# Performance work log

Measured on AMD Instinct MI355X. Metric: run time of the kernel, lower is better.

## Reference

```python
import jax, jax.numpy as jnp
import numpy as np

B = 4096
D_IN = 1024
D_H = 1024


def setup_inputs() -> dict:
    key = jax.random.key(0)
    ks = jax.random.split(key, 11)
    s = 1.0 / np.sqrt(D_IN + D_H)  # torch nn.Linear default init scale
    def w(k):
        return jax.random.uniform(k, (D_H, D_IN + D_H), jnp.float32, -s, s)
    def b(k):
        return jax.random.uniform(k, (D_H,), jnp.float32, -s, s)
    return {
        "inputs": jax.random.normal(ks[0], (B, D_IN), jnp.float32),
        "h_prev": jax.random.normal(ks[1], (B, D_H), jnp.float32),
        "c_prev": jax.random.normal(ks[2], (B, D_H), jnp.float32),
        "W_i": w(ks[3]), "b_i": b(ks[4]),
        "W_f": w(ks[5]), "b_f": b(ks[6]),
        "W_c": w(ks[7]), "b_c": b(ks[8]),
        "W_o": w(ks[9]), "b_o": b(ks[10]),
    }


def reference(inputs, h_prev, c_prev, W_i, b_i, W_f, b_f, W_c, b_c, W_o, b_o):
    combined = jnp.concatenate([inputs, h_prev], axis=1)  # [B, D_IN+D_H]
    # Fuse the four gate projections into one GEMM: [B, 4*D_H]
    W = jnp.concatenate([W_i, W_f, W_c, W_o], axis=0)      # [4*D_H, D_IN+D_H]
    bvec = jnp.concatenate([b_i, b_f, b_c, b_o], axis=0)   # [4*D_H]
    z = combined @ W.T + bvec
    zi, zf, zc, zo = jnp.split(z, 4, axis=1)
    i_gate = jax.nn.sigmoid(zi)
    f_gate = jax.nn.sigmoid(zf)
    c_gate = jnp.tanh(zc)
    o_gate = jax.nn.sigmoid(zo)
    c_next = f_gate * c_prev + i_gate * c_gate
    h_next = o_gate * jnp.tanh(c_next)
    return (h_next, c_next)
```

## Files before the change

### kernel.cpp

```cpp
#include <hip/hip_runtime.h>
#include <hip/hip_bf16.h>
#include <stdint.h>

#define B_SZ 4096
#define D_K  2048
#define DH   1024

#define BM 128
#define BN_H 32
#define BK 64

typedef __attribute__((ext_vector_type(8))) short short8;
typedef __attribute__((ext_vector_type(4))) float floatx4;

__device__ __forceinline__ float fast_sigmoid(float x) {
  return 1.0f / (1.0f + __expf(-x));
}
__device__ __forceinline__ float fast_tanh(float x) {
  return 2.0f / (1.0f + __expf(-2.0f * x)) - 1.0f;
}

__device__ __forceinline__ uint32_t bf16pk(float a, float b) {
  union { float f; uint32_t u; } ua, ub;
  ua.f = a; ub.f = b;
  uint32_t x = ua.u + (0x7FFFu + ((ua.u >> 16) & 1u));
  uint32_t y = ub.u + (0x7FFFu + ((ub.u >> 16) & 1u));
  return (x >> 16) | (y & 0xFFFF0000u);
}

__global__ __launch_bounds__(256) void prep_kernel(
    const float* __restrict__ xin, const float* __restrict__ hprev,
    const float* __restrict__ Wi, const float* __restrict__ Wf,
    const float* __restrict__ Wc, const float* __restrict__ Wo,
    uint32_t* __restrict__ Abf, uint32_t* __restrict__ Wbf)
{
  const int NT = (B_SZ * D_K) / 8;
  int t = blockIdx.x * blockDim.x + threadIdx.x;
  const float* src;
  uint32_t* dst;
  if (t < NT) {
    int idx8 = t * 8;
    int m = idx8 >> 11;
    int k = idx8 & (D_K - 1);
    src = (k < 1024) ? (xin + m * 1024 + k) : (hprev + m * 1024 + (k - 1024));
    dst = Abf + t * 4;
  } else {
    int u = t - NT;
    int idx8 = u * 8;
    int n = idx8 >> 11;
    int k = idx8 & (D_K - 1);
    int g = n >> 10, h = n & 1023;
    const float* wsrc = (g == 0) ? Wi : (g == 1) ? Wf : (g == 2) ? Wc : Wo;
    src = wsrc + (size_t)h * D_K + k;
    dst = Wbf + u * 4;
  }
  float4 f0 = *(const float4*)(src);
  float4 f1 = *(const float4*)(src + 4);
  uint4 v;
  v.x = bf16pk(f0.x, f0.y);
  v.y = bf16pk(f0.z, f0.w);
  v.z = bf16pk(f1.x, f1.y);
  v.w = bf16pk(f1.z, f1.w);
  *(uint4*)dst = v;
}

__global__ __launch_bounds__(256, 3) void lstm_gemm_kernel(
    const __hip_bfloat16* __restrict__ A,
    const __hip_bfloat16* __restrict__ W,
    const float* __restrict__ bi, const float* __restrict__ bfv,
    const float* __restrict__ bc, const float* __restrict__ bo,
    const float* __restrict__ cprev,
    float* __restrict__ out)
{
  __shared__ __align__(16) __hip_bfloat16 lA[BM * BK];
  __shared__ __align__(16) __hip_bfloat16 lB[128 * BK];

  const int m0 = blockIdx.x * BM;
  const int h0 = blockIdx.y * BN_H;
  const int tid = threadIdx.x;
  const int wave = tid >> 6;
  const int lane = tid & 63;
  const int wm = wave >> 1;
  const int wn = wave & 1;

  const int sr = lane >> 3;
  const int pc = lane & 7;
  const int gc = pc ^ sr;

  const __hip_bfloat16* aSrc[4];
  const __hip_bfloat16* bSrc[4];
  __hip_bfloat16* aDst[4];
  __hip_bfloat16* bDst[4];
  #pragma unroll
  for (int j = 0; j < 4; ++j) {
    int row = j * 32 + wave * 8 + sr;
    aSrc[j] = A + (size_t)(m0 + row) * D_K + gc * 8;
    aDst[j] = &lA[row * BK + pc * 8];
    bSrc[j] = W + (size_t)(j * DH + h0 + wave * 8 + sr) * D_K + gc * 8;
    bDst[j] = &lB[row * BK + pc * 8];
  }

  floatx4 acc[4][4];
  #pragma unroll
  for (int i = 0; i < 4; ++i)
    #pragma unroll
    for (int j = 0; j < 4; ++j)
      acc[i][j] = (floatx4){0.f, 0.f, 0.f, 0.f};

  const int fr = lane & 15;
  const int q  = lane >> 4;
  const int key = fr & 7;
  const int cx0 = ((q + 0) ^ key) * 8;
  const int cx1 = ((q + 4) ^ key) * 8;

  for (int kt = 0; kt < D_K; kt += BK) {
    #pragma unroll
    for (int j = 0; j < 4; ++j)
      __builtin_amdgcn_global_load_lds(
          (const __attribute__((address_space(1))) void*)(aSrc[j] + kt),
          (__attribute__((address_space(3))) void*)aDst[j], 16, 0, 0);
    #pragma unroll
    for (int j = 0; j < 4; ++j)
      __builtin_amdgcn_global_load_lds(
          (const __attribute__((address_space(1))) void*)(bSrc[j] + kt),
          (__attribute__((address_space(3))) void*)bDst[j], 16, 0, 0);
    __syncthreads();

    #pragma unroll
    for (int kk = 0; kk < 2; ++kk) {
      const int cx = kk ? cx1 : cx0;
      short8 bfr[4];
      #pragma unroll
      for (int g = 0; g < 4; ++g)
        bfr[g] = *(const short8*)&lB[(g * 32 + wn * 16 + fr) * BK + cx];
      #pragma unroll
      for (int i = 0; i < 4; ++i) {
        short8 af = *(const short8*)&lA[(wm * 64 + i * 16 + fr) * BK + cx];
        acc[i][0] = __builtin_amdgcn_mfma_f32_16x16x32_bf16(af, bfr[0], acc[i][0], 0, 0, 0);
        acc[i][1] = __builtin_amdgcn_mfma_f32_16x16x32_bf16(af, bfr[1], acc[i][1], 0, 0, 0);
        acc[i][2] = __builtin_amdgcn_mfma_f32_16x16x32_bf16(af, bfr[2], acc[i][2], 0, 0, 0);
        acc[i][3] = __builtin_amdgcn_mfma_f32_16x16x32_bf16(af, bfr[3], acc[i][3], 0, 0, 0);
      }
    }
    __syncthreads();
  }

  const int col = lane & 15;
  const int rq = lane >> 4;
  const int h = h0 + wn * 16 + col;
  const float bias_i = bi[h], bias_f = bfv[h], bias_c = bc[h], bias_o = bo[h];
  float* hout = out;
  float* cout = out + (size_t)B_SZ * DH;
  #pragma unroll
  for (int i = 0; i < 4; ++i) {
    int mb = m0 + wm * 64 + i * 16 + rq * 4;
    #pragma unroll
    for (int r = 0; r < 4; ++r) {
      int m = mb + r;
      float zi = acc[i][0][r] + bias_i;
      float zf = acc[i][1][r] + bias_f;
      float zc = acc[i][2][r] + bias_c;
      float zo = acc[i][3][r] + bias_o;
      float ig = fast_sigmoid(zi);
      float fg = fast_sigmoid(zf);
      float cg = fast_tanh(zc);
      float og = fast_sigmoid(zo);
      float cp = cprev[(size_t)m * DH + h];
      float cn = fg * cp + ig * cg;
      float hn = og * fast_tanh(cn);
      hout[(size_t)m * DH + h] = hn;
      cout[(size_t)m * DH + h] = cn;
    }
  }
}

extern "C" void kernel_launch(void* const* d_in, const int* in_sizes, int n_in,
                              void* d_out, int out_size, void* d_ws, size_t ws_size,
                              hipStream_t stream)
{
  const float* xin   = (const float*)d_in[0];
  const float* hprev = (const float*)d_in[1];
  const float* cprev = (const float*)d_in[2];
  const float* Wi    = (const float*)d_in[3];
  const float* bi    = (const float*)d_in[4];
  const float* Wf    = (const float*)d_in[5];
  const float* bfv   = (const float*)d_in[6];
  const float* Wc    = (const float*)d_in[7];
  const float* bc    = (const float*)d_in[8];
  const float* Wo    = (const float*)d_in[9];
  const float* bo    = (const float*)d_in[10];
  float* out = (float*)d_out;

  __hip_bfloat16* Abf = (__hip_bfloat16*)d_ws;
  __hip_bfloat16* Wbf = Abf + (size_t)B_SZ * D_K;

  const int totalThreads = 2 * (B_SZ * D_K / 8);
  prep_kernel<<<totalThreads / 256, 256, 0, stream>>>(
      xin, hprev, Wi, Wf, Wc, Wo, (uint32_t*)Abf, (uint32_t*)Wbf);

  dim3 grid(B_SZ / BM, DH / BN_H);
  lstm_gemm_kernel<<<grid, 256, 0, stream>>>(Abf, Wbf, bi, bfv, bc, bo, cprev, out);
}
```

Before: 208.4 us.

## Double-buffer LDS tiles with BK=32 and remap blocks for XCD locality

```diff
diff --git a/kernel.cpp b/kernel.cpp
--- a/kernel.cpp
+++ b/kernel.cpp
@@ -8,7 +8,7 @@
 
 #define BM 128
 #define BN_H 32
-#define BK 64
+#define BK 32
 
 typedef __attribute__((ext_vector_type(8))) short short8;
 typedef __attribute__((ext_vector_type(4))) float floatx4;
@@ -34,34 +34,32 @@
     const float* __restrict__ Wc, const float* __restrict__ Wo,
     uint32_t* __restrict__ Abf, uint32_t* __restrict__ Wbf)
 {
-  const int NT = (B_SZ * D_K) / 8;
+  const int NT = (B_SZ * D_K) / 4;
   int t = blockIdx.x * blockDim.x + threadIdx.x;
   const float* src;
   uint32_t* dst;
   if (t < NT) {
-    int idx8 = t * 8;
-    int m = idx8 >> 11;
-    int k = idx8 & (D_K - 1);
-    src = (k < 1024) ? (xin + m * 1024 + k) : (hprev + m * 1024 + (k - 1024));
-    dst = Abf + t * 4;
+    int idx4 = t * 4;
+    int m = idx4 >> 11;
+    int k = idx4 & (D_K - 1);
+    src = (k < 1024) ? (xin + (size_t)m * 1024 + k)
+                     : (hprev + (size_t)m * 1024 + (k - 1024));
+    dst = Abf + (size_t)t * 2;
   } else {
     int u = t - NT;
-    int idx8 = u * 8;
-    int n = idx8 >> 11;
-    int k = idx8 & (D_K - 1);
+    int idx4 = u * 4;
+    int n = idx4 >> 11;
+    int k = idx4 & (D_K - 1);
     int g = n >> 10, h = n & 1023;
     const float* wsrc = (g == 0) ? Wi : (g == 1) ? Wf : (g == 2) ? Wc : Wo;
     src = wsrc + (size_t)h * D_K + k;
-    dst = Wbf + u * 4;
-  }
-  float4 f0 = *(const float4*)(src);
-  float4 f1 = *(const float4*)(src + 4);
-  uint4 v;
-  v.x = bf16pk(f0.x, f0.y);
-  v.y = bf16pk(f0.z, f0.w);
-  v.z = bf16pk(f1.x, f1.y);
-  v.w = bf16pk(f1.z, f1.w);
-  *(uint4*)dst = v;
+    dst = Wbf + (size_t)u * 2;
+  }
+  float4 f = *(const float4*)src;
+  uint2 v;
+  v.x = bf16pk(f.x, f.y);
+  v.y = bf16pk(f.z, f.w);
+  *(uint2*)dst = v;
 }
 
 __global__ __launch_bounds__(256, 3) void lstm_gemm_kernel(
@@ -72,32 +70,36 @@
     const float* __restrict__ cprev,
     float* __restrict__ out)
 {
-  __shared__ __align__(16) __hip_bfloat16 lA[BM * BK];
-  __shared__ __align__(16) __hip_bfloat16 lB[128 * BK];
-
-  const int m0 = blockIdx.x * BM;
-  const int h0 = blockIdx.y * BN_H;
+  __shared__ __align__(16) __hip_bfloat16 lA[2][BM * BK];
+  __shared__ __align__(16) __hip_bfloat16 lB[2][128 * BK];
+
+  const int l = blockIdx.x;
+  const int q = l >> 3;
+  const int mIdx = q & 31;
+  const int hIdx = (l & 7) * 4 + (q >> 5);
+  const int m0 = mIdx * BM;
+  const int h0 = hIdx * BN_H;
+
   const int tid = threadIdx.x;
   const int wave = tid >> 6;
   const int lane = tid & 63;
   const int wm = wave >> 1;
   const int wn = wave & 1;
 
-  const int sr = lane >> 3;
-  const int pc = lane & 7;
-  const int gc = pc ^ sr;
-
-  const __hip_bfloat16* aSrc[4];
-  const __hip_bfloat16* bSrc[4];
-  __hip_bfloat16* aDst[4];
-  __hip_bfloat16* bDst[4];
-  #pragma unroll
-  for (int j = 0; j < 4; ++j) {
-    int row = j * 32 + wave * 8 + sr;
+  const int sr = lane >> 2;
+  const int pc = lane & 3;
+  const int gc = pc ^ ((sr >> 1) & 3);
+
+  const __hip_bfloat16* aSrc[2];
+  const __hip_bfloat16* bSrc[2];
+  int aOff[2], bOff[2];
+  #pragma unroll
+  for (int j = 0; j < 2; ++j) {
+    int row = j * 64 + wave * 16 + sr;
     aSrc[j] = A + (size_t)(m0 + row) * D_K + gc * 8;
-    aDst[j] = &lA[row * BK + pc * 8];
-    bSrc[j] = W + (size_t)(j * DH + h0 + wave * 8 + sr) * D_K + gc * 8;
-    bDst[j] = &lB[row * BK + pc * 8];
+    aOff[j] = row * BK + pc * 8;
+    bSrc[j] = W + (size_t)((row >> 5) * DH + h0 + (row & 31)) * D_K + gc * 8;
+    bOff[j] = row * BK + pc * 8;
   }
 
   floatx4 acc[4][4];
@@ -108,41 +110,52 @@
       acc[i][j] = (floatx4){0.f, 0.f, 0.f, 0.f};
 
   const int fr = lane & 15;
-  const int q  = lane >> 4;
-  const int key = fr & 7;
-  const int cx0 = ((q + 0) ^ key) * 8;
-  const int cx1 = ((q + 4) ^ key) * 8;
-
-  for (int kt = 0; kt < D_K; kt += BK) {
-    #pragma unroll
-    for (int j = 0; j < 4; ++j)
-      __builtin_amdgcn_global_load_lds(
-          (const __attribute__((address_space(1))) void*)(aSrc[j] + kt),
-          (__attribute__((address_space(3))) void*)aDst[j], 16, 0, 0);
-    #pragma unroll
-    for (int j = 0; j < 4; ++j)
-      __builtin_amdgcn_global_load_lds(
-          (const __attribute__((address_space(1))) void*)(bSrc[j] + kt),
-          (__attribute__((address_space(3))) void*)bDst[j], 16, 0, 0);
-    __syncthreads();
-
-    #pragma unroll
-    for (int kk = 0; kk < 2; ++kk) {
-      const int cx = kk ? cx1 : cx0;
-      short8 bfr[4];
+  const int kq = lane >> 4;
+  const int cx = ((kq ^ ((fr >> 1) & 3)) * 8);
+
+  const int NITER = D_K / BK;
+
+  #pragma unroll
+  for (int j = 0; j < 2; ++j) {
+    __builtin_amdgcn_global_load_lds(
+        (const __attribute__((address_space(1))) void*)(aSrc[j]),
+        (__attribute__((address_space(3))) void*)&lA[0][aOff[j]], 16, 0, 0);
+    __builtin_amdgcn_global_load_lds(
+        (const __attribute__((address_space(1))) void*)(bSrc[j]),
+        (__attribute__((address_space(3))) void*)&lB[0][bOff[j]], 16, 0, 0);
+  }
+  __syncthreads();
+
+  int p = 0;
+  for (int kt = 0; kt < NITER; ++kt) {
+    if (kt + 1 < NITER) {
+      const int koff = (kt + 1) * BK;
       #pragma unroll
-      for (int g = 0; g < 4; ++g)
-        bfr[g] = *(const short8*)&lB[(g * 32 + wn * 16 + fr) * BK + cx];
-      #pragma unroll
-      for (int i = 0; i < 4; ++i) {
-        short8 af = *(const short8*)&lA[(wm * 64 + i * 16 + fr) * BK + cx];
-        acc[i][0] = __builtin_amdgcn_mfma_f32_16x16x32_bf16(af, bfr[0], acc[i][0], 0, 0, 0);
-        acc[i][1] = __builtin_amdgcn_mfma_f32_16x16x32_bf16(af, bfr[1], acc[i][1], 0, 0, 0);
-        acc[i][2] = __builtin_amdgcn_mfma_f32_16x16x32_bf16(af, bfr[2], acc[i][2], 0, 0, 0);
-        acc[i][3] = __builtin_amdgcn_mfma_f32_16x16x32_bf16(af, bfr[3], acc[i][3], 0, 0, 0);
+      for (int j = 0; j < 2; ++j) {
+        __builtin_amdgcn_global_load_lds(
+            (const __attribute__((address_space(1))) void*)(aSrc[j] + koff),
+            (__attribute__((address_space(3))) void*)&lA[p ^ 1][aOff[j]], 16, 0, 0);
+        __builtin_amdgcn_global_load_lds(
+            (const __attribute__((address_space(1))) void*)(bSrc[j] + koff),
+            (__attribute__((address_space(3))) void*)&lB[p ^ 1][bOff[j]], 16, 0, 0);
       }
     }
+
+    short8 bfr[4];
+    #pragma unroll
+    for (int g = 0; g < 4; ++g)
+      bfr[g] = *(const short8*)&lB[p][(g * 32 + wn * 16 + fr) * BK + cx];
+    #pragma unroll
+    for (int i = 0; i < 4; ++i) {
+      short8 af = *(const short8*)&lA[p][(wm * 64 + i * 16 + fr) * BK + cx];
+      acc[i][0] = __builtin_amdgcn_mfma_f32_16x16x32_bf16(af, bfr[0], acc[i][0], 0, 0, 0);
+      acc[i][1] = __builtin_amdgcn_mfma_f32_16x16x32_bf16(af, bfr[1], acc[i][1], 0, 0, 0);
+      acc[i][2] = __builtin_amdgcn_mfma_f32_16x16x32_bf16(af, bfr[2], acc[i][2], 0, 0, 0);
+      acc[i][3] = __builtin_amdgcn_mfma_f32_16x16x32_bf16(af, bfr[3], acc[i][3], 0, 0, 0);
+    }
+
     __syncthreads();
+    p ^= 1;
   }
 
   const int col = lane & 15;
@@ -194,10 +207,10 @@
   __hip_bfloat16* Abf = (__hip_bfloat16*)d_ws;
   __hip_bfloat16* Wbf = Abf + (size_t)B_SZ * D_K;
 
-  const int totalThreads = 2 * (B_SZ * D_K / 8);
+  const int totalThreads = 2 * (B_SZ * D_K / 4);
   prep_kernel<<<totalThreads / 256, 256, 0, stream>>>(
       xin, hprev, Wi, Wf, Wc, Wo, (uint32_t*)Abf, (uint32_t*)Wbf);
 
-  dim3 grid(B_SZ / BM, DH / BN_H);
-  lstm_gemm_kernel<<<grid, 256, 0, stream>>>(Abf, Wbf, bi, bfv, bc, bo, cprev, out);
-}
+  lstm_gemm_kernel<<<dim3(1024), 256, 0, stream>>>(
+      Abf, Wbf, bi, bfv, bc, bo, cprev, out);
+}
```

Measured after the change: 221.1 us. +6.1%, slower.
